# Optimization experiments

Hardware: AMD Instinct MI355X
Metric: run time of the kernel (lower is better)

The kernel has to match this reference:

```python
import jax, jax.numpy as jnp
import numpy as np

N_ANCHORS = 200000
TOPK = 4096          # pre-NMS top-k (standard detector practice, fixed output shape)
CONF_T = 0.5
IOU_T = 0.6


def setup_inputs() -> dict:
    key = jax.random.key(0)
    k1, k2, k3 = jax.random.split(key, 3)
    # build valid xyxy boxes: random centers in a 1024x1024 image, sizes 4..128
    cxcy = jax.random.uniform(k1, (1, N_ANCHORS, 2), minval=0.0, maxval=1024.0)
    wh = jax.random.uniform(k2, (1, N_ANCHORS, 2), minval=4.0, maxval=128.0)
    boxes = jnp.concatenate([cxcy - wh / 2, cxcy + wh / 2], axis=-1)  # [1,N,4]
    confs = jax.random.uniform(k3, (1, N_ANCHORS))                    # [1,N]
    return {"boxes": boxes, "confs": confs}


def _pairwise_iou(b):
    # b: [K,4] xyxy -> iou: [K,K]
    area = jnp.clip(b[:, 2] - b[:, 0], 0.0) * jnp.clip(b[:, 3] - b[:, 1], 0.0)
    lt = jnp.maximum(b[:, None, :2], b[None, :, :2])
    rb = jnp.minimum(b[:, None, 2:], b[None, :, 2:])
    wh = jnp.clip(rb - lt, 0.0)
    inter = wh[..., 0] * wh[..., 1]
    return inter / (area[:, None] + area[None, :] - inter + 1e-9)


def reference(boxes, confs):
    b = boxes[0]          # [N,4] single batch (module is single-batch single-class)
    c = confs[0]          # [N]
    # confidence threshold mask; invalid scores pushed below any valid score
    scores = jnp.where(c >= CONF_T, c, -1.0)
    top_scores, idx = jax.lax.top_k(scores, TOPK)   # sorted descending
    top_boxes = b[idx]                              # [K,4]
    iou = _pairwise_iou(top_boxes)                  # [K,K]
    valid_k = top_scores >= CONF_T

    # greedy sequential NMS over score-sorted candidates
    def body(i, state):
        keep, sup = state
        is_keep = jnp.logical_not(sup[i])
        keep = keep.at[i].set(is_keep)
        sup = sup | (is_keep & (iou[i] > IOU_T))
        return (keep, sup)

    keep0 = jnp.zeros((TOPK,), dtype=bool)
    keep, _ = jax.lax.fori_loop(0, TOPK, body, (keep0, jnp.logical_not(valid_k)))

    # [K,5] = x1,y1,x2,y2,conf ; suppressed rows zeroed (fixed output shape)
    out = jnp.concatenate([top_boxes, top_scores[:, None]], axis=-1)
    return jnp.where(keep[:, None], out, 0.0)
```

## Files before the change

kernel.cpp:

```cpp
#include <hip/hip_runtime.h>

#define NTOP   4096
#define SORTN  8192
#define CONF_T 0.5f
#define IOU_T  0.6f

#define HIST_OFF   0
#define CUT_OFF    8192
#define CNT_OFF    8196
#define COMP_OFF   16384
#define MEMSET_BYTES 81920
#define KEYS_OFF   131072
#define TB_OFF     2097152
#define TC_OFF     2162688
#define VALID_OFF  2179072
#define KEEP_OFF   2179584
#define MASK_OFF   4194304

typedef unsigned long long u64;
typedef unsigned int u32;

__global__ void k_keys(const float* __restrict__ confs, u64* __restrict__ keys,
                       u32* __restrict__ hist, int n) {
    int i = blockIdx.x * 256 + threadIdx.x;
    if (i >= n) return;
    float s = confs[i];
    if (s >= CONF_T) {
        u32 u = __float_as_uint(s);
        keys[i] = ((u64)u << 32) | (u32)(~i);
        int bin = (int)(u >> 12) - 0x3F000;
        bin = bin < 0 ? 0 : (bin > 2047 ? 2047 : bin);
        atomicAdd(&hist[bin], 1u);
    } else {
        keys[i] = 0ull;
    }
}

__global__ __launch_bounds__(256) void k_findcut(const u32* __restrict__ hist,
                                                 int* __restrict__ cut) {
    __shared__ u32 ch[256];
    int t = threadIdx.x;
    u32 h[8]; u32 s = 0;
#pragma unroll
    for (int k = 0; k < 8; ++k) { h[k] = hist[t * 8 + k]; s += h[k]; }
    ch[t] = s;
    __syncthreads();
    for (int off = 1; off < 256; off <<= 1) {
        u32 v = ch[t];
        u32 add = (t + off < 256) ? ch[t + off] : 0u;
        __syncthreads();
        ch[t] = v + add;
        __syncthreads();
    }
    u32 incl = ch[t];
    u32 above = incl - s;
    if (above < NTOP && incl >= NTOP) {
        u32 cum = above; int c = 0;
        for (int k = 7; k >= 0; --k) {
            cum += h[k];
            if (cum >= NTOP) { c = t * 8 + k; break; }
        }
        *cut = c;
    }
    if (t == 0 && ch[0] < NTOP) *cut = 0;
}

__global__ void k_compact(const u64* __restrict__ keys, const int* __restrict__ cut,
                          u64* __restrict__ comp, u32* __restrict__ counter, int n) {
    int i = blockIdx.x * 256 + threadIdx.x;
    if (i >= n) return;
    u64 key = keys[i];
    if (!key) return;
    int bin = (int)(u32)(key >> 44) - 0x3F000;
    bin = bin < 0 ? 0 : (bin > 2047 ? 2047 : bin);
    if (bin >= *cut) {
        u32 p = atomicAdd(counter, 1u);
        if (p < SORTN) comp[p] = key;
    }
}

__global__ __launch_bounds__(1024) void k_sort(const u64* __restrict__ comp,
                                               const float4* __restrict__ boxes,
                                               float4* __restrict__ tb,
                                               float* __restrict__ tc,
                                               u64* __restrict__ validmask) {
    __shared__ u64 sm[SORTN];
    int t = threadIdx.x;
    for (int i = t; i < SORTN; i += 1024) sm[i] = comp[i];
    __syncthreads();
    for (int k = 2; k <= SORTN; k <<= 1) {
        for (int j = k >> 1; j > 0; j >>= 1) {
            for (int i = t; i < SORTN; i += 1024) {
                int ixj = i ^ j;
                if (ixj > i) {
                    u64 a = sm[i], b = sm[ixj];
                    bool sw = ((i & k) == 0) ? (a < b) : (a > b);
                    if (sw) { sm[i] = b; sm[ixj] = a; }
                }
            }
            __syncthreads();
        }
    }
    for (int base = 0; base < NTOP; base += 1024) {
        int k = base + t;
        u64 key = sm[k];
        float score = __uint_as_float((u32)(key >> 32));
        bool valid = (key != 0ull) && (score >= CONF_T);
        float4 b = make_float4(0.f, 0.f, 0.f, 0.f);
        if (valid) {
            u32 idx = ~(u32)(key & 0xFFFFFFFFull);
            b = boxes[idx];
        }
        tb[k] = b;
        tc[k] = score;
        u64 bal = __ballot(valid);
        if ((t & 63) == 0) validmask[k >> 6] = bal;
    }
}

__global__ __launch_bounds__(256) void k_mask(const float4* __restrict__ tb,
                                              u64* __restrict__ mask) {
    __shared__ float4 cb[64];
    __shared__ float  ca[64];
    int w = blockIdx.x;
    int t = threadIdx.x;
    if (t < 64) {
        float4 b = tb[w * 64 + t];
        cb[t] = b;
        ca[t] = fmaxf(b.z - b.x, 0.f) * fmaxf(b.w - b.y, 0.f);
    }
    __syncthreads();
    int row = blockIdx.y * 256 + t;
    float4 rb = tb[row];
    float ra = fmaxf(rb.z - rb.x, 0.f) * fmaxf(rb.w - rb.y, 0.f);
    u64 m = 0;
#pragma unroll 8
    for (int j = 0; j < 64; ++j) {
        float4 c = cb[j];
        float lx = fmaxf(rb.x, c.x), ly = fmaxf(rb.y, c.y);
        float rx = fminf(rb.z, c.z), ry = fminf(rb.w, c.w);
        float iw = fmaxf(rx - lx, 0.f), ih = fmaxf(ry - ly, 0.f);
        float inter = iw * ih;
        float iou = inter / (ra + ca[j] - inter + 1e-9f);
        if (iou > IOU_T) m |= (1ull << j);
    }
    mask[(size_t)row * 64 + w] = m;
}

__global__ __launch_bounds__(64, 1) void k_nms(const u64* __restrict__ mask,
                                               const u64* __restrict__ validmask,
                                               u64* __restrict__ keep) {
    int lane = threadIdx.x;
    u64 mysup = ~validmask[lane];
    u64 mykeep = 0;

    u64 pf[32];
#pragma unroll
    for (int d = 0; d < 32; ++d) pf[d] = mask[(size_t)d * 64 + lane];

    for (int w = 0; w < 64; ++w) {
        u32 clo = (u32)__builtin_amdgcn_readlane((int)(u32)mysup, w);
        u32 chi = (u32)__builtin_amdgcn_readlane((int)(u32)(mysup >> 32), w);
        u64 cur = ((u64)chi << 32) | clo;
        u64 blockkeep = 0;
#pragma unroll
        for (int sub = 0; sub < 64; sub += 32) {
#pragma unroll
            for (int d = 0; d < 32; ++d) {
                int i = (w << 6) + sub + d;
                int nxt = i + 32; if (nxt >= NTOP) nxt = i;
                u64 rowv = pf[d];
                pf[d] = mask[(size_t)nxt * 64 + lane];
                u32 dlo = (u32)__builtin_amdgcn_readlane((int)(u32)rowv, w);
                u32 dhi = (u32)__builtin_amdgcn_readlane((int)(u32)(rowv >> 32), w);
                u64 dwv = ((u64)dhi << 32) | dlo;
                const int bit = sub + d;
                bool is_keep = ((cur >> bit) & 1ull) == 0ull;
                u64 m = is_keep ? ~0ull : 0ull;
                cur |= dwv & m;
                mysup |= rowv & m;
                blockkeep |= is_keep ? (1ull << bit) : 0ull;
            }
        }
        if (lane == w) mykeep = blockkeep;
    }
    keep[lane] = mykeep;
}

__global__ void k_out(const float4* __restrict__ tb, const float* __restrict__ tc,
                      const u64* __restrict__ keep, float* __restrict__ out) {
    int k = blockIdx.x * 256 + threadIdx.x;
    bool kp = (keep[k >> 6] >> (k & 63)) & 1ull;
    float4 b = tb[k];
    float c = tc[k];
    float* o = out + (size_t)k * 5;
    o[0] = kp ? b.x : 0.f;
    o[1] = kp ? b.y : 0.f;
    o[2] = kp ? b.z : 0.f;
    o[3] = kp ? b.w : 0.f;
    o[4] = kp ? c : 0.f;
}

extern "C" void kernel_launch(void* const* d_in, const int* in_sizes, int n_in,
                              void* d_out, int out_size, void* d_ws, size_t ws_size,
                              hipStream_t stream) {
    const float4* boxes = (const float4*)d_in[0];
    const float*  confs = (const float*)d_in[1];
    float* out = (float*)d_out;
    char* ws = (char*)d_ws;
    int n = in_sizes[1];

    u32* hist    = (u32*)(ws + HIST_OFF);
    int* cut     = (int*)(ws + CUT_OFF);
    u32* counter = (u32*)(ws + CNT_OFF);
    u64* comp    = (u64*)(ws + COMP_OFF);
    u64* keys    = (u64*)(ws + KEYS_OFF);
    float4* tb   = (float4*)(ws + TB_OFF);
    float*  tc   = (float*)(ws + TC_OFF);
    u64* validm  = (u64*)(ws + VALID_OFF);
    u64* keep    = (u64*)(ws + KEEP_OFF);
    u64* mask    = (u64*)(ws + MASK_OFF);

    hipMemsetAsync(ws, 0, MEMSET_BYTES, stream);
    k_keys<<<(n + 255) / 256, 256, 0, stream>>>(confs, keys, hist, n);
    k_findcut<<<1, 256, 0, stream>>>(hist, cut);
    k_compact<<<(n + 255) / 256, 256, 0, stream>>>(keys, cut, comp, counter, n);
    k_sort<<<1, 1024, 0, stream>>>(comp, boxes, tb, tc, validm);
    k_mask<<<dim3(64, 16), 256, 0, stream>>>(tb, mask);
    k_nms<<<1, 64, 0, stream>>>(mask, validm, keep);
    k_out<<<16, 256, 0, stream>>>(tb, tc, keep, out);
}
```

Before: 431.3 us.

## Warp-specialize NMS with producer warps double-buffering mask blocks in LDS

```diff
diff --git a/kernel.cpp b/kernel.cpp
--- a/kernel.cpp
+++ b/kernel.cpp
@@ -147,44 +147,75 @@
     mask[(size_t)row * 64 + w] = m;
 }
 
-__global__ __launch_bounds__(64, 1) void k_nms(const u64* __restrict__ mask,
-                                               const u64* __restrict__ validmask,
-                                               u64* __restrict__ keep) {
-    int lane = threadIdx.x;
-    u64 mysup = ~validmask[lane];
-    u64 mykeep = 0;
-
-    u64 pf[32];
-#pragma unroll
-    for (int d = 0; d < 32; ++d) pf[d] = mask[(size_t)d * 64 + lane];
-
-    for (int w = 0; w < 64; ++w) {
-        u32 clo = (u32)__builtin_amdgcn_readlane((int)(u32)mysup, w);
-        u32 chi = (u32)__builtin_amdgcn_readlane((int)(u32)(mysup >> 32), w);
-        u64 cur = ((u64)chi << 32) | clo;
-        u64 blockkeep = 0;
-#pragma unroll
-        for (int sub = 0; sub < 64; sub += 32) {
-#pragma unroll
-            for (int d = 0; d < 32; ++d) {
-                int i = (w << 6) + sub + d;
-                int nxt = i + 32; if (nxt >= NTOP) nxt = i;
-                u64 rowv = pf[d];
-                pf[d] = mask[(size_t)nxt * 64 + lane];
-                u32 dlo = (u32)__builtin_amdgcn_readlane((int)(u32)rowv, w);
-                u32 dhi = (u32)__builtin_amdgcn_readlane((int)(u32)(rowv >> 32), w);
-                u64 dwv = ((u64)dhi << 32) | dlo;
-                const int bit = sub + d;
-                bool is_keep = ((cur >> bit) & 1ull) == 0ull;
-                u64 m = is_keep ? ~0ull : 0ull;
-                cur |= dwv & m;
-                mysup |= rowv & m;
-                blockkeep |= is_keep ? (1ull << bit) : 0ull;
+#define RD(p, base) \
+    p##0 = Bp[(base + 0) * 64 + lane]; p##1 = Bp[(base + 1) * 64 + lane]; \
+    p##2 = Bp[(base + 2) * 64 + lane]; p##3 = Bp[(base + 3) * 64 + lane]; \
+    p##4 = Bp[(base + 4) * 64 + lane]; p##5 = Bp[(base + 5) * 64 + lane]; \
+    p##6 = Bp[(base + 6) * 64 + lane]; p##7 = Bp[(base + 7) * 64 + lane];
+
+#define ST(rv, bit) { \
+    u32 dlo = (u32)__builtin_amdgcn_readlane((int)(u32)(rv), w); \
+    u32 dhi = (u32)__builtin_amdgcn_readlane((int)(u32)((rv) >> 32), w); \
+    u64 dwv = ((u64)dhi << 32) | dlo;    \
+    bool is_keep = ((cur >> (bit)) & 1ull) == 0ull; \
+    u64 mm = is_keep ? ~0ull : 0ull;     \
+    cur |= dwv & mm;                     \
+    mysup |= (rv) & mm;                  \
+    blockkeep |= is_keep ? (1ull << (bit)) : 0ull; }
+
+#define PR(p, base) \
+    ST(p##0, base + 0) ST(p##1, base + 1) ST(p##2, base + 2) ST(p##3, base + 3) \
+    ST(p##4, base + 4) ST(p##5, base + 5) ST(p##6, base + 6) ST(p##7, base + 7)
+
+__global__ __launch_bounds__(256, 1) void k_nms(const u64* __restrict__ mask,
+                                                const u64* __restrict__ validmask,
+                                                u64* __restrict__ keep) {
+    __shared__ u64 buf[2][64 * 64];
+    int tid = threadIdx.x;
+    int lane = tid & 63;
+    int wid = tid >> 6;
+
+    {
+        const ulonglong2* src = (const ulonglong2*)mask;
+        ulonglong2* dst = (ulonglong2*)buf[0];
+        for (int k = tid; k < 2048; k += 256) dst[k] = src[k];
+    }
+
+    u64 mysup = 0, mykeep = 0;
+    if (wid == 0) mysup = ~validmask[lane];
+    __syncthreads();
+
+    for (int b = 0; b < 64; ++b) {
+        if (wid != 0) {
+            if (b + 1 < 64) {
+                const ulonglong2* src = (const ulonglong2*)(mask + (size_t)(b + 1) * 4096);
+                ulonglong2* dst = (ulonglong2*)buf[(b & 1) ^ 1];
+                int p = tid - 64;
+                for (int k = p; k < 2048; k += 192) dst[k] = src[k];
             }
-        }
-        if (lane == w) mykeep = blockkeep;
-    }
-    keep[lane] = mykeep;
+        } else {
+            const u64* Bp = buf[b & 1];
+            int w = b;
+            u32 clo = (u32)__builtin_amdgcn_readlane((int)(u32)mysup, w);
+            u32 chi = (u32)__builtin_amdgcn_readlane((int)(u32)(mysup >> 32), w);
+            u64 cur = ((u64)chi << 32) | clo;
+            u64 blockkeep = 0;
+            u64 x0, x1, x2, x3, x4, x5, x6, x7;
+            u64 y0, y1, y2, y3, y4, y5, y6, y7;
+            RD(x, 0)
+            RD(y, 8)  PR(x, 0)
+            RD(x, 16) PR(y, 8)
+            RD(y, 24) PR(x, 16)
+            RD(x, 32) PR(y, 24)
+            RD(y, 40) PR(x, 32)
+            RD(x, 48) PR(y, 40)
+            RD(y, 56) PR(x, 48)
+            PR(y, 56)
+            if (lane == w) mykeep = blockkeep;
+        }
+        __syncthreads();
+    }
+    if (wid == 0) keep[lane] = mykeep;
 }
 
 __global__ void k_out(const float4* __restrict__ tb, const float* __restrict__ tc,
@@ -227,6 +258,6 @@
     k_compact<<<(n + 255) / 256, 256, 0, stream>>>(keys, cut, comp, counter, n);
     k_sort<<<1, 1024, 0, stream>>>(comp, boxes, tb, tc, validm);
     k_mask<<<dim3(64, 16), 256, 0, stream>>>(tb, mask);
-    k_nms<<<1, 64, 0, stream>>>(mask, validm, keep);
+    k_nms<<<1, 256, 0, stream>>>(mask, validm, keep);
     k_out<<<16, 256, 0, stream>>>(tb, tc, keep, out);
 }
```

Result: slower. 468.9 us (+8.7%).
